# Optimization experiments

Hardware: AMD Instinct MI355X
Metric: run time of the kernel (lower is better)

## Reference

```python
import jax, jax.numpy as jnp
import numpy as np

N = 50000      # nodes
E = 500000     # edges
IN = 256       # input feature dim
HID = 64       # hidden (per-head) dim, layer 1
H1 = 4         # heads, layer 1
NC = 64        # num_classes (layer 2 out, 1 head)
ED = 32        # edge_dim
T = 8          # num_etypes
SLOPE = 0.2    # leakyrelu negative slope


def setup_inputs() -> dict:
    key = jax.random.key(0)
    ks = jax.random.split(key, 20)
    p = lambda k, shape: (jax.random.normal(k, shape, jnp.float32) * 0.05)
    return {
        "h": jax.random.normal(ks[0], (N, IN), jnp.float32),
        "row": jax.random.randint(ks[1], (E,), 0, N, jnp.int32),   # src
        "col": jax.random.randint(ks[2], (E,), 0, N, jnp.int32),   # dst
        "etype": jax.random.randint(ks[3], (E,), 0, T, jnp.int32),
        # layer 1 (4 heads, no residual, elu activation)
        "edge_emb1": p(ks[4], (T, ED)),
        "W1": p(ks[5], (IN, HID * H1)),
        "Wr1": p(ks[6], (T, ED, ED * H1)),      # TypedLinear per-etype weight
        "a_l1": p(ks[7], (H1, HID)),
        "a_r1": p(ks[8], (H1, HID)),
        "a_e1": p(ks[9], (H1, ED)),
        # layer 2 (1 head, residual Linear, no activation)
        "edge_emb2": p(ks[10], (T, ED)),
        "W2": p(ks[11], (HID * H1, NC)),
        "Wr2": p(ks[12], (T, ED, ED)),
        "a_l2": p(ks[13], (1, NC)),
        "a_r2": p(ks[14], (1, NC)),
        "a_e2": p(ks[15], (1, ED)),
        "res_W2": p(ks[16], (HID * H1, NC)),
        "res_b2": p(ks[17], (NC,)),
    }


def _simple_hgn_conv(h, row, col, etype, edge_emb, W, Wr, a_l, a_r, a_e,
                     res_W, res_b, apply_act):
    """One SimpleHGNConv layer. h:[N,in], returns [N, out_dim*H] (D-major, H-minor
    layout, matching emb.permute(0,2,1).view in the torch code)."""
    H, D = a_l.shape            # num_heads, out_dim
    n = h.shape[0]
    emb = (h @ W).reshape(n, H, D)                     # [N,H,D]
    emb = jnp.where(jnp.isnan(emb), 0.0, emb)
    # TypedLinear: edge_emb[etype] @ Wr[etype]; only T distinct rows -> per-type GEMM
    ee = jnp.einsum('te,teo->to', edge_emb, Wr).reshape(T, H, ED)  # [T,H,ED]
    h_l = jnp.einsum('nhd,hd->nh', emb, a_l)[row]      # [E,H]
    h_r = jnp.einsum('nhd,hd->nh', emb, a_r)[col]      # [E,H]
    h_e = jnp.einsum('thd,hd->th', ee, a_e)[etype]     # [E,H]
    att = jax.nn.leaky_relu(h_l + h_r + h_e, SLOPE)    # [E,H]
    # edge_softmax: normalize over incoming edges of each destination node (col)
    seg_max = jax.ops.segment_max(att, col, num_segments=n)   # [N,H]
    att = jnp.exp(att - seg_max[col])
    seg_sum = jax.ops.segment_sum(att, col, num_segments=n)   # [N,H]
    alpha = att / seg_sum[col]                          # [E,H]
    # u_mul_e + sum aggregation
    msg = emb[row] * alpha[:, :, None]                  # [E,H,D]
    out = jax.ops.segment_sum(msg, col, num_segments=n) # [N,H,D]
    out = out.transpose(0, 2, 1).reshape(n, D * H)      # D-major layout
    if res_W is not None:
        out = out + h @ res_W + res_b
    if apply_act:
        out = jax.nn.elu(out)
    return out


def reference(h, row, col, etype,
              edge_emb1, W1, Wr1, a_l1, a_r1, a_e1,
              edge_emb2, W2, Wr2, a_l2, a_r2, a_e2, res_W2, res_b2):
    h1 = _simple_hgn_conv(h, row, col, etype, edge_emb1, W1, Wr1,
                          a_l1, a_r1, a_e1, None, None, True)
    h2 = _simple_hgn_conv(h1, row, col, etype, edge_emb2, W2, Wr2,
                          a_l2, a_r2, a_e2, res_W2, res_b2, False)
    # split by node type (first half type 'l', second half type 'v')
    return (h2[: N // 2], h2[N // 2 :])
```

## Files before the change

### kernel.cpp

```cpp
#include <hip/hip_runtime.h>
#include <hip/hip_bf16.h>

typedef __bf16 bf16x8 __attribute__((ext_vector_type(8)));
typedef float f32x4 __attribute__((ext_vector_type(4)));

#define IN_DIM 256
#define NT 8

__device__ __forceinline__ float b2f(unsigned short u) {
  union { unsigned int i; float f; } x; x.i = ((unsigned int)u) << 16; return x.f;
}
__device__ __forceinline__ float lo2f(unsigned int w) {
  union { unsigned int i; float f; } x; x.i = w << 16; return x.f;
}
__device__ __forceinline__ float hi2f(unsigned int w) {
  union { unsigned int i; float f; } x; x.i = w & 0xFFFF0000u; return x.f;
}
__device__ __forceinline__ unsigned short f2b(float f) {
  union { float f; unsigned int i; } u; u.f = f;
  unsigned int r = u.i + 0x7FFF + ((u.i >> 16) & 1);
  return (unsigned short)(r >> 16);
}
__device__ __forceinline__ float lrelu(float x) { return x >= 0.f ? x : 0.2f * x; }
__device__ __forceinline__ float ldf(const void* p, size_t i, int isf32) {
  return isf32 ? ((const float*)p)[i] : b2f(((const unsigned short*)p)[i]);
}

__global__ void detect_kernel(const unsigned int* __restrict__ hw, int* __restrict__ flag) {
  int tid = threadIdx.x;
  int bad = 0;
  for (int i = 0; i < 4; i++) {
    unsigned int w = hw[tid * 4 + i];
    unsigned int e = (w & 0x7FFFu) >> 7;
    if (e >= 0xC0u) bad++;
  }
#pragma unroll
  for (int off = 32; off; off >>= 1) bad += __shfl_xor(bad, off);
  if (tid == 0) *flag = (bad > 8) ? 1 : 0;
}

__global__ void prep_all_kernel(const void* __restrict__ W1, const void* __restrict__ W2,
                                const void* __restrict__ rW2,
                                const void* __restrict__ al1, const void* __restrict__ ar1,
                                const void* __restrict__ al2, const void* __restrict__ ar2,
                                const void* __restrict__ ee1, const void* __restrict__ Wr1,
                                const void* __restrict__ ae1,
                                const void* __restrict__ ee2, const void* __restrict__ Wr2,
                                const void* __restrict__ ae2,
                                unsigned short* __restrict__ W1t,
                                unsigned short* __restrict__ W2t,
                                float* __restrict__ a2l, float* __restrict__ a2r,
                                float* __restrict__ he1, float* __restrict__ he2,
                                float* __restrict__ alD, float* __restrict__ arD,
                                const int* __restrict__ dflag) {
  int isf32 = *dflag;
  int b = blockIdx.x, tid = threadIdx.x;
  if (b < 384) {
    int j = b, k = tid;
    if (j < 256) {
      int src = (j & 3) * 64 + (j >> 2);
      W1t[j * 256 + k] = f2b(ldf(W1, (size_t)k * 256 + src, isf32));
    } else {
      int o = j - 256;
      float v = (o < 64) ? ldf(W2, (size_t)k * 64 + o, isf32)
                         : ldf(rW2, (size_t)k * 64 + (o - 64), isf32);
      W2t[o * 256 + k] = f2b(v);
    }
  } else if (b < 448) {
    int k = (b - 384) * 4 + (tid >> 6), d = tid & 63;
    float w2 = ldf(W2, (size_t)k * 64 + d, isf32);
    float l2 = w2 * ldf(al2, d, isf32);
    float r2 = w2 * ldf(ar2, d, isf32);
#pragma unroll
    for (int off = 32; off; off >>= 1) { l2 += __shfl_xor(l2, off); r2 += __shfl_xor(r2, off); }
    if (d == 0) { a2l[k] = l2; a2r[k] = r2; }
  } else {
    int bid = b - 448;
    int t = tid >> 5, d = tid & 31;
    if (bid < 4) {
      int h = bid;
      float s = 0.f;
#pragma unroll
      for (int e = 0; e < 32; e++)
        s += ldf(ee1, t * 32 + e, isf32) * ldf(Wr1, (size_t)(t * 32 + e) * 128 + h * 32 + d, isf32);
      float v = s * ldf(ae1, h * 32 + d, isf32);
#pragma unroll
      for (int off = 16; off; off >>= 1) v += __shfl_xor(v, off);
      if (d == 0) he1[t * 4 + h] = v;
    } else if (bid == 4) {
      float s = 0.f;
#pragma unroll
      for (int e = 0; e < 32; e++)
        s += ldf(ee2, t * 32 + e, isf32) * ldf(Wr2, (size_t)(t * 32 + e) * 32 + d, isf32);
      float v = s * ldf(ae2, d, isf32);
#pragma unroll
      for (int off = 16; off; off >>= 1) v += __shfl_xor(v, off);
      if (d == 0) he2[t] = v;
    } else {
      int j = tid;
      alD[j] = ldf(al1, (j & 3) * 64 + (j >> 2), isf32);
      arD[j] = ldf(ar1, (j & 3) * 64 + (j >> 2), isf32);
    }
  }
}

__global__ __launch_bounds__(256, 2) void gemm1_fused(
    const void* __restrict__ A, int M,
    const unsigned short* __restrict__ Bt,
    unsigned short* __restrict__ emb1,
    const float* __restrict__ alD, const float* __restrict__ arD,
    float* __restrict__ hl1, float* __restrict__ hr1,
    const int* __restrict__ dflag) {
  __shared__ unsigned short As[64 * 64];
  __shared__ unsigned short Bs[256 * 64];
  __shared__ float lsum[4][64][4];
  __shared__ float rsum[4][64][4];
  int isf32 = *dflag;
  const int tid = threadIdx.x;
  const int m0 = blockIdx.x * 64;
  const int wv = tid >> 6, lane = tid & 63;
  const int q = lane >> 4, m = lane & 15;
  const int jp = wv * 64;
  f32x4 acc[4][4] = {};
  for (int kc = 0; kc < 256; kc += 64) {
    {
      int row = tid >> 2, qt = tid & 3;
      int gr = m0 + row;
      unsigned short tmp[16];
      if (gr < M) {
        if (isf32) {
          const float* ap = (const float*)A + (size_t)gr * 256 + kc + qt * 16;
          float4 v0 = *(const float4*)ap;
          float4 v1 = *(const float4*)(ap + 4);
          float4 v2 = *(const float4*)(ap + 8);
          float4 v3 = *(const float4*)(ap + 12);
          tmp[0]=f2b(v0.x); tmp[1]=f2b(v0.y); tmp[2]=f2b(v0.z); tmp[3]=f2b(v0.w);
          tmp[4]=f2b(v1.x); tmp[5]=f2b(v1.y); tmp[6]=f2b(v1.z); tmp[7]=f2b(v1.w);
          tmp[8]=f2b(v2.x); tmp[9]=f2b(v2.y); tmp[10]=f2b(v2.z); tmp[11]=f2b(v2.w);
          tmp[12]=f2b(v3.x); tmp[13]=f2b(v3.y); tmp[14]=f2b(v3.z); tmp[15]=f2b(v3.w);
        } else {
          const unsigned short* ap = (const unsigned short*)A + (size_t)gr * 256 + kc + qt * 16;
          *(int4*)tmp = *(const int4*)ap;
          *(int4*)(tmp + 8) = *(const int4*)(ap + 8);
        }
      } else {
        for (int x = 0; x < 16; x++) tmp[x] = 0;
      }
      int g0 = (qt * 2) ^ (row & 7);
      int g1 = (qt * 2 + 1) ^ (row & 7);
      *(int4*)(As + row * 64 + g0 * 8) = *(int4*)tmp;
      *(int4*)(As + row * 64 + g1 * 8) = *(int4*)(tmp + 8);
    }
    {
#pragma unroll
      for (int i = 0; i < 8; i++) {
        int id = tid + i * 256;
        int row = id >> 3, gg = id & 7;
        int4 v = *(const int4*)(Bt + (size_t)row * 256 + kc + gg * 8);
        int pg = gg ^ (row & 7);
        *(int4*)(Bs + row * 64 + pg * 8) = v;
      }
    }
    __syncthreads();
#pragma unroll
    for (int ks = 0; ks < 2; ks++) {
      int gk = ks * 4 + q;
      bf16x8 afr[4];
#pragma unroll
      for (int cm = 0; cm < 4; cm++) {
        int row = cm * 16 + m;
        afr[cm] = *(const bf16x8*)(As + row * 64 + (gk ^ (row & 7)) * 8);
      }
#pragma unroll
      for (int cj = 0; cj < 4; cj++) {
        int jr = jp + cj * 16 + m;
        bf16x8 b = *(const bf16x8*)(Bs + jr * 64 + (gk ^ (jr & 7)) * 8);
#pragma unroll
        for (int cm = 0; cm < 4; cm++)
          acc[cm][cj] = __builtin_amdgcn_mfma_f32_16x16x32_bf16(afr[cm], b, acc[cm][cj], 0, 0, 0);
      }
    }
    __syncthreads();
  }
  float al[4], ar[4];
#pragma unroll
  for (int cj = 0; cj < 4; cj++) {
    al[cj] = alD[jp + cj * 16 + m];
    ar[cj] = arD[jp + cj * 16 + m];
  }
#pragma unroll
  for (int cm = 0; cm < 4; cm++) {
#pragma unroll
    for (int r = 0; r < 4; r++) {
      int lrow = cm * 16 + q * 4 + r;
      int gm = m0 + lrow;
      float lp = 0.f, rp = 0.f;
#pragma unroll
      for (int cj = 0; cj < 4; cj++) {
        float v = acc[cm][cj][r];
        if (gm < M) emb1[(size_t)gm * 256 + jp + cj * 16 + m] = f2b(v);
        lp += v * al[cj]; rp += v * ar[cj];
      }
      lp += __shfl_xor(lp, 4); lp += __shfl_xor(lp, 8);
      rp += __shfl_xor(rp, 4); rp += __shfl_xor(rp, 8);
      if (m < 4) { lsum[wv][lrow][m] = lp; rsum[wv][lrow][m] = rp; }
    }
  }
  __syncthreads();
  {
    int row = tid >> 2, h = tid & 3;
    int gm = m0 + row;
    if (gm < M) {
      float l = lsum[0][row][h] + lsum[1][row][h] + lsum[2][row][h] + lsum[3][row][h];
      float r = rsum[0][row][h] + rsum[1][row][h] + rsum[2][row][h] + rsum[3][row][h];
      hl1[(size_t)gm * 4 + h] = l;
      hr1[(size_t)gm * 4 + h] = r;
    }
  }
}

__global__ __launch_bounds__(256, 2) void gemm2_fused(
    const unsigned short* __restrict__ A, int M,
    const unsigned short* __restrict__ Bt,
    unsigned short* __restrict__ emb2, unsigned short* __restrict__ res,
    const void* __restrict__ bias, const int* __restrict__ dflag) {
  __shared__ unsigned short As[64 * 64];
  __shared__ unsigned short Bs[128 * 64];
  int isf32 = *dflag;
  const int tid = threadIdx.x;
  const int m0 = blockIdx.x * 64;
  const int wv = tid >> 6, lane = tid & 63;
  const int q = lane >> 4, m = lane & 15;
  const int jp = (wv & 1) * 64;
  const int mh = (wv >> 1) * 32;
  f32x4 acc[2][4] = {};
  for (int kc = 0; kc < 256; kc += 64) {
    {
      int row = tid >> 2, qt = tid & 3;
      int gr = m0 + row;
      unsigned short tmp[16];
      if (gr < M) {
        const unsigned short* ap = A + (size_t)gr * 256 + kc + qt * 16;
        *(int4*)tmp = *(const int4*)ap;
        *(int4*)(tmp + 8) = *(const int4*)(ap + 8);
      } else {
        for (int x = 0; x < 16; x++) tmp[x] = 0;
      }
      int g0 = (qt * 2) ^ (row & 7);
      int g1 = (qt * 2 + 1) ^ (row & 7);
      *(int4*)(As + row * 64 + g0 * 8) = *(int4*)tmp;
      *(int4*)(As + row * 64 + g1 * 8) = *(int4*)(tmp + 8);
    }
    {
#pragma unroll
      for (int i = 0; i < 4; i++) {
        int id = tid + i * 256;
        int row = id >> 3, gg = id & 7;
        int4 v = *(const int4*)(Bt + (size_t)row * 256 + kc + gg * 8);
        int pg = gg ^ (row & 7);
        *(int4*)(Bs + row * 64 + pg * 8) = v;
      }
    }
    __syncthreads();
#pragma unroll
    for (int ks = 0; ks < 2; ks++) {
      int gk = ks * 4 + q;
      bf16x8 afr[2];
#pragma unroll
      for (int cm = 0; cm < 2; cm++) {
        int row = mh + cm * 16 + m;
        afr[cm] = *(const bf16x8*)(As + row * 64 + (gk ^ (row & 7)) * 8);
      }
#pragma unroll
      for (int cj = 0; cj < 4; cj++) {
        int jr = jp + cj * 16 + m;
        bf16x8 b = *(const bf16x8*)(Bs + jr * 64 + (gk ^ (jr & 7)) * 8);
#pragma unroll
        for (int cm = 0; cm < 2; cm++)
          acc[cm][cj] = __builtin_amdgcn_mfma_f32_16x16x32_bf16(afr[cm], b, acc[cm][cj], 0, 0, 0);
      }
    }
    __syncthreads();
  }
  float bv[4];
#pragma unroll
  for (int cj = 0; cj < 4; cj++)
    bv[cj] = (jp == 64) ? ldf(bias, cj * 16 + m, isf32) : 0.f;
#pragma unroll
  for (int cm = 0; cm < 2; cm++) {
#pragma unroll
    for (int r = 0; r < 4; r++) {
      int gm = m0 + mh + cm * 16 + q * 4 + r;
      if (gm < M) {
#pragma unroll
        for (int cj = 0; cj < 4; cj++) {
          float v = acc[cm][cj][r];
          int gj = cj * 16 + m;
          if (jp == 0) emb2[(size_t)gm * 64 + gj] = f2b(v);
          else res[(size_t)gm * 64 + gj] = f2b(v + bv[cj]);
        }
      }
    }
  }
}

__global__ void count_kernel(const int* __restrict__ col, int* __restrict__ cnt,
                             int E_, int N_) {
  int e = blockIdx.x * 256 + threadIdx.x;
  if (e >= E_) return;
  int c = col[e];
  if ((unsigned)c < (unsigned)N_) atomicAdd(&cnt[c], 1);
}

__global__ void scan1_kernel(const int* __restrict__ cnt, int* __restrict__ ptrb,
                             int* __restrict__ bsum, int n) {
  __shared__ int wsum[4];
  int tid = threadIdx.x, lane = tid & 63, wid = tid >> 6;
  int i = blockIdx.x * 256 + tid;
  int v = (i < n) ? cnt[i] : 0;
  int x = v;
#pragma unroll
  for (int off = 1; off < 64; off <<= 1) {
    int y = __shfl_up(x, off);
    if (lane >= off) x += y;
  }
  if (lane == 63) wsum[wid] = x;
  __syncthreads();
  int woff = 0;
#pragma unroll
  for (int k = 0; k < 4; k++) woff += (k < wid) ? wsum[k] : 0;
  if (i < n) ptrb[i] = x - v + woff;
  if (tid == 255) bsum[blockIdx.x] = woff + x;
}

__global__ void scan2_kernel(int* __restrict__ bsum, int* __restrict__ ptrb,
                             int nb, int n) {
  __shared__ int wsum[4];
  int tid = threadIdx.x, lane = tid & 63, wid = tid >> 6;
  int v = (tid < nb) ? bsum[tid] : 0;
  int x = v;
#pragma unroll
  for (int off = 1; off < 64; off <<= 1) {
    int y = __shfl_up(x, off);
    if (lane >= off) x += y;
  }
  if (lane == 63) wsum[wid] = x;
  __syncthreads();
  int woff = 0;
#pragma unroll
  for (int k = 0; k < 4; k++) woff += (k < wid) ? wsum[k] : 0;
  if (tid < nb) bsum[tid] = x - v + woff;
  if (tid == 255) ptrb[n] = woff + x;
}

__global__ void scan3_kernel(int* __restrict__ ptrb, const int* __restrict__ bsum, int n) {
  int i = blockIdx.x * 256 + threadIdx.x;
  if (i < n) ptrb[i] += bsum[blockIdx.x];
}

__global__ void fill_kernel(const int* __restrict__ col, const int* __restrict__ row,
                            const int* __restrict__ ety, const int* __restrict__ ptrb,
                            int* __restrict__ cnt, int* __restrict__ srcc, int E_, int N_) {
  int e = blockIdx.x * 256 + threadIdx.x;
  if (e >= E_) return;
  int c = col[e];
  if ((unsigned)c >= (unsigned)N_) return;
  int pos = atomicSub(&cnt[c], 1) - 1;
  long long slot = (long long)ptrb[c] + pos;
  if (slot >= 0 && slot < E_) {
    int sr = row[e], t = ety[e];
    srcc[slot] = ((unsigned)sr < (unsigned)N_ && (unsigned)t < (unsigned)NT)
                     ? (sr | (t << 20)) : -1;
  }
}

__global__ __launch_bounds__(256) void agg1_kernel(
    const int* __restrict__ ptrb, const int* __restrict__ srcc,
    const float* __restrict__ hl1, const float* __restrict__ hr1,
    const float* __restrict__ he1,
    const unsigned short* __restrict__ emb1, unsigned short* __restrict__ h1,
    const float* __restrict__ a2l, const float* __restrict__ a2r,
    float* __restrict__ hl2, float* __restrict__ hr2,
    int N_, int E_) {
  __shared__ float4 wds[4][64];
  __shared__ int sds[4][64];
  int wv = threadIdx.x >> 6, lane = threadIdx.x & 63;
  int node = blockIdx.x * 4 + wv;
  if (node >= N_) return;
  int p0 = ptrb[node], p1 = ptrb[node + 1];
  p0 = max(0, min(p0, E_)); p1 = max(p0, min(p1, E_));
  float4 hrv = *(const float4*)(hr1 + 4 * (size_t)node);
  float s0 = 0.f, s1 = 0.f, s2 = 0.f, s3 = 0.f;
  float acc[8] = {0.f,0.f,0.f,0.f,0.f,0.f,0.f,0.f};
  int g = lane >> 5, sub = lane & 31;
  for (int pb = p0; pb < p1; pb += 64) {
    int mc = p1 - pb; if (mc > 64) mc = 64;
    float4 w = {0.f, 0.f, 0.f, 0.f};
    int src = 0;
    if (lane < mc) {
      int spk = srcc[pb + lane];
      if (spk >= 0) {
        int sr = spk & 0xFFFFF, t = spk >> 20;
        float4 a = *(const float4*)(hl1 + 4 * (size_t)sr);
        float4 gg = *(const float4*)(he1 + 4 * (size_t)t);
        w.x = __expf(lrelu(a.x + hrv.x + gg.x));
        w.y = __expf(lrelu(a.y + hrv.y + gg.y));
        w.z = __expf(lrelu(a.z + hrv.z + gg.z));
        w.w = __expf(lrelu(a.w + hrv.w + gg.w));
        src = sr;
      }
    }
    s0 += w.x; s1 += w.y; s2 += w.z; s3 += w.w;
    wds[wv][lane] = w;
    sds[wv][lane] = src;
    for (int j = 0; j < mc; j += 4) {
      int jj0 = j + g, jj1 = j + 2 + g;
      bool v0 = jj0 < mc, v1 = jj1 < mc;
      float4 u0, u1; int r0 = 0, r1 = 0;
      int4 raw0, raw1;
      if (v0) { u0 = wds[wv][jj0]; r0 = sds[wv][jj0];
                raw0 = *(const int4*)(emb1 + (size_t)r0 * 256 + sub * 8); }
      if (v1) { u1 = wds[wv][jj1]; r1 = sds[wv][jj1];
                raw1 = *(const int4*)(emb1 + (size_t)r1 * 256 + sub * 8); }
      if (v0) {
        acc[0] += u0.x * lo2f(raw0.x); acc[1] += u0.y * hi2f(raw0.x);
        acc[2] += u0.z * lo2f(raw0.y); acc[3] += u0.w * hi2f(raw0.y);
        acc[4] += u0.x * lo2f(raw0.z); acc[5] += u0.y * hi2f(raw0.z);
        acc[6] += u0.z * lo2f(raw0.w); acc[7] += u0.w * hi2f(raw0.w);
      }
      if (v1) {
        acc[0] += u1.x * lo2f(raw1.x); acc[1] += u1.y * hi2f(raw1.x);
        acc[2] += u1.z * lo2f(raw1.y); acc[3] += u1.w * hi2f(raw1.y);
        acc[4] += u1.x * lo2f(raw1.z); acc[5] += u1.y * hi2f(raw1.z);
        acc[6] += u1.z * lo2f(raw1.w); acc[7] += u1.w * hi2f(raw1.w);
      }
    }
  }
#pragma unroll
  for (int off = 32; off; off >>= 1) {
    s0 += __shfl_xor(s0, off); s1 += __shfl_xor(s1, off);
    s2 += __shfl_xor(s2, off); s3 += __shfl_xor(s3, off);
  }
#pragma unroll
  for (int k = 0; k < 8; k++) acc[k] += __shfl_xor(acc[k], 32);
  float lp = 0.f, rp = 0.f;
  if (g == 0) {
    float sv[4] = {s0, s1, s2, s3};
    unsigned short o[8];
#pragma unroll
    for (int k = 0; k < 8; k++) {
      float r = (sv[k & 3] > 0.f) ? acc[k] / sv[k & 3] : 0.f;
      r = r > 0.f ? r : __expf(r) - 1.f;
      o[k] = f2b(r);
      int j = sub * 8 + k;
      lp += r * a2l[j];
      rp += r * a2r[j];
    }
    *(int4*)(h1 + (size_t)node * 256 + sub * 8) = *(int4*)o;
  }
#pragma unroll
  for (int off = 1; off < 32; off <<= 1) { lp += __shfl_xor(lp, off); rp += __shfl_xor(rp, off); }
  if (lane == 0) { hl2[node] = lp; hr2[node] = rp; }
}

__global__ __launch_bounds__(256) void agg2_kernel(
    const int* __restrict__ ptrb, const int* __restrict__ srcc,
    const float* __restrict__ hl2, const float* __restrict__ hr2,
    const float* __restrict__ he2,
    const unsigned short* __restrict__ emb2, const unsigned short* __restrict__ res,
    void* __restrict__ out, int N_, int E_, const int* __restrict__ dflag) {
  __shared__ int2 wsd[4][64];
  int isf32 = *dflag;
  int wv = threadIdx.x >> 6, lane = threadIdx.x & 63;
  int node = blockIdx.x * 4 + wv;
  if (node >= N_) return;
  int p0 = ptrb[node], p1 = ptrb[node + 1];
  p0 = max(0, min(p0, E_)); p1 = max(p0, min(p1, E_));
  float hrv = hr2[node];
  float s = 0.f;
  float acc[4] = {0.f, 0.f, 0.f, 0.f};
  int g = lane >> 4, sub = lane & 15;
  for (int pb = p0; pb < p1; pb += 64) {
    int mc = p1 - pb; if (mc > 64) mc = 64;
    float w = 0.f;
    int src = 0;
    if (lane < mc) {
      int spk = srcc[pb + lane];
      if (spk >= 0) {
        int sr = spk & 0xFFFFF, t = spk >> 20;
        w = __expf(lrelu(hl2[sr] + hrv + he2[t]));
        src = sr;
      }
    }
    s += w;
    int2 pk; pk.x = __float_as_int(w); pk.y = src;
    wsd[wv][lane] = pk;
    for (int j = 0; j < mc; j += 8) {
      int jj0 = j + g, jj1 = j + 4 + g;
      bool v0 = jj0 < mc, v1 = jj1 < mc;
      float u0, u1; int r0 = 0, r1 = 0;
      int2 raw0, raw1;
      if (v0) { int2 ws = wsd[wv][jj0]; u0 = __int_as_float(ws.x); r0 = ws.y;
                raw0 = *(const int2*)(emb2 + (size_t)r0 * 64 + sub * 4); }
      if (v1) { int2 ws = wsd[wv][jj1]; u1 = __int_as_float(ws.x); r1 = ws.y;
                raw1 = *(const int2*)(emb2 + (size_t)r1 * 64 + sub * 4); }
      if (v0) {
        acc[0] += u0 * lo2f(raw0.x); acc[1] += u0 * hi2f(raw0.x);
        acc[2] += u0 * lo2f(raw0.y); acc[3] += u0 * hi2f(raw0.y);
      }
      if (v1) {
        acc[0] += u1 * lo2f(raw1.x); acc[1] += u1 * hi2f(raw1.x);
        acc[2] += u1 * lo2f(raw1.y); acc[3] += u1 * hi2f(raw1.y);
      }
    }
  }
#pragma unroll
  for (int off = 32; off; off >>= 1) s += __shfl_xor(s, off);
#pragma unroll
  for (int k = 0; k < 4; k++) {
    acc[k] += __shfl_xor(acc[k], 16);
    acc[k] += __shfl_xor(acc[k], 32);
  }
  if (g == 0) {
    ushort4 rv = *(const ushort4*)(res + (size_t)node * 64 + sub * 4);
    float o0 = ((s > 0.f) ? acc[0] / s : 0.f) + b2f(rv.x);
    float o1 = ((s > 0.f) ? acc[1] / s : 0.f) + b2f(rv.y);
    float o2 = ((s > 0.f) ? acc[2] / s : 0.f) + b2f(rv.z);
    float o3 = ((s > 0.f) ? acc[3] / s : 0.f) + b2f(rv.w);
    size_t oi = (size_t)node * 64 + sub * 4;
    if (isf32) {
      float4 ov = {o0, o1, o2, o3};
      *(float4*)((float*)out + oi) = ov;
    } else {
      ushort4 ov; ov.x = f2b(o0); ov.y = f2b(o1); ov.z = f2b(o2); ov.w = f2b(o3);
      *(ushort4*)((unsigned short*)out + oi) = ov;
    }
  }
}

extern "C" void kernel_launch(void* const* d_in, const int* in_sizes, int n_in,
                              void* d_out, int out_size, void* d_ws, size_t ws_size,
                              hipStream_t stream) {
  const int N = in_sizes[0] / IN_DIM;
  const int E = in_sizes[1];

  const void* h   = d_in[0];
  const int* row  = (const int*)d_in[1];
  const int* col  = (const int*)d_in[2];
  const int* ety  = (const int*)d_in[3];
  const void* ee1 = d_in[4];
  const void* W1  = d_in[5];
  const void* Wr1 = d_in[6];
  const void* al1 = d_in[7];
  const void* ar1 = d_in[8];
  const void* ae1 = d_in[9];
  const void* ee2 = d_in[10];
  const void* W2  = d_in[11];
  const void* Wr2 = d_in[12];
  const void* al2 = d_in[13];
  const void* ar2 = d_in[14];
  const void* ae2 = d_in[15];
  const void* rW2 = d_in[16];
  const void* rb2 = d_in[17];

  char* p = (char*)d_ws;
  auto take = [&](size_t b) { char* q = p; p += (b + 255) & ~(size_t)255; return q; };
  unsigned short* h1   = (unsigned short*)take((size_t)N * 256 * 2);
  unsigned short* emb1 = (unsigned short*)take((size_t)N * 256 * 2);
  int* srcc = (int*)take((size_t)E * 4);
  int* ptrb = (int*)take((size_t)(N + 1) * 4);
  int* cnt  = (int*)take((size_t)N * 4);
  int* bsum = (int*)take(1024);
  float* hl1 = (float*)take((size_t)N * 4 * 4);
  float* hr1 = (float*)take((size_t)N * 4 * 4);
  float* hl2 = (float*)take((size_t)N * 4);
  float* hr2 = (float*)take((size_t)N * 4);
  unsigned short* W1t = (unsigned short*)take(256 * 256 * 2);
  unsigned short* W2t = (unsigned short*)take(128 * 256 * 2);
  float* a2l = (float*)take(256 * 4);
  float* a2r = (float*)take(256 * 4);
  float* alD = (float*)take(256 * 4);
  float* arD = (float*)take(256 * 4);
  float* he1 = (float*)take(NT * 4 * 4);
  float* he2 = (float*)take(NT * 4);
  int* dflag = (int*)take(256);
  unsigned short* emb2 = emb1;
  unsigned short* res  = emb1 + (size_t)N * 64;

  const size_t need = (size_t)(p - (char*)d_ws);
  if (need > ws_size) {
    hipMemsetAsync(d_out, 0, (size_t)out_size * 2, stream);
    return;
  }

  const int EB = (E + 255) / 256;
  const int MB = (N + 63) / 64;
  const int SB = (N + 255) / 256;

  detect_kernel<<<1, 64, 0, stream>>>((const unsigned int*)h, dflag);
  hipMemsetAsync(cnt, 0, (size_t)N * 4, stream);
  prep_all_kernel<<<454, 256, 0, stream>>>(W1, W2, rW2, al1, ar1, al2, ar2,
                                           ee1, Wr1, ae1, ee2, Wr2, ae2,
                                           W1t, W2t, a2l, a2r, he1, he2, alD, arD, dflag);

  count_kernel<<<EB, 256, 0, stream>>>(col, cnt, E, N);
  scan1_kernel<<<SB, 256, 0, stream>>>(cnt, ptrb, bsum, N);
  scan2_kernel<<<1, 256, 0, stream>>>(bsum, ptrb, SB, N);
  scan3_kernel<<<SB, 256, 0, stream>>>(ptrb, bsum, N);
  fill_kernel<<<EB, 256, 0, stream>>>(col, row, ety, ptrb, cnt, srcc, E, N);

  gemm1_fused<<<MB, 256, 0, stream>>>(h, N, W1t, emb1, alD, arD, hl1, hr1, dflag);
  agg1_kernel<<<(N + 3) / 4, 256, 0, stream>>>(
      ptrb, srcc, hl1, hr1, he1, emb1, h1, a2l, a2r, hl2, hr2, N, E);

  gemm2_fused<<<MB, 256, 0, stream>>>(h1, N, W2t, emb2, res, rb2, dflag);
  agg2_kernel<<<(N + 3) / 4, 256, 0, stream>>>(
      ptrb, srcc, hl2, hr2, he2, emb2, res, d_out, N, E, dflag);
}
```

Baseline: 284.5 us.

## Map four destination nodes per wavefront in both aggregation kernels

Both aggregation kernels now assign 16 lanes per destination node, so one wavefront handles four nodes instead of one. This targets the lane waste seen with average degree around 10, where most of a 64-wide edge chunk sat idle, and drops the cross-half shuffle reductions. Each lane now gathers 32 bytes of bf16 per edge in agg1 and keeps 16 accumulators. In exchange, register pressure rises and nodes in the same wave with unequal degree cause divergence through the __any loop.

```diff
diff --git a/kernel.cpp b/kernel.cpp
--- a/kernel.cpp
+++ b/kernel.cpp
@@ -384,83 +384,121 @@
     int N_, int E_) {
   __shared__ float4 wds[4][64];
   __shared__ int sds[4][64];
-  int wv = threadIdx.x >> 6, lane = threadIdx.x & 63;
-  int node = blockIdx.x * 4 + wv;
-  if (node >= N_) return;
-  int p0 = ptrb[node], p1 = ptrb[node + 1];
-  p0 = max(0, min(p0, E_)); p1 = max(p0, min(p1, E_));
-  float4 hrv = *(const float4*)(hr1 + 4 * (size_t)node);
+  const int tid = threadIdx.x;
+  const int wv = tid >> 6, lane = tid & 63;
+  const int g = lane >> 4, ln = lane & 15;
+  const int node = blockIdx.x * 16 + wv * 4 + g;
+  const bool nv = node < N_;
+  int p0 = 0, p1 = 0;
+  if (nv) {
+    p0 = ptrb[node]; p1 = ptrb[node + 1];
+    p0 = max(0, min(p0, E_)); p1 = max(p0, min(p1, E_));
+  }
+  float4 hrv = {0.f, 0.f, 0.f, 0.f};
+  if (nv) hrv = *(const float4*)(hr1 + 4 * (size_t)node);
   float s0 = 0.f, s1 = 0.f, s2 = 0.f, s3 = 0.f;
-  float acc[8] = {0.f,0.f,0.f,0.f,0.f,0.f,0.f,0.f};
-  int g = lane >> 5, sub = lane & 31;
-  for (int pb = p0; pb < p1; pb += 64) {
-    int mc = p1 - pb; if (mc > 64) mc = 64;
+  float acc[16];
+#pragma unroll
+  for (int k = 0; k < 16; k++) acc[k] = 0.f;
+  const unsigned short* erow = emb1 + ln * 16;
+  for (int pb = p0;; pb += 16) {
+    if (!__any(pb < p1)) break;
+    int mc = (pb < p1) ? min(p1 - pb, 16) : 0;
     float4 w = {0.f, 0.f, 0.f, 0.f};
     int src = 0;
-    if (lane < mc) {
-      int spk = srcc[pb + lane];
+    if (ln < mc) {
+      int spk = srcc[pb + ln];
       if (spk >= 0) {
         int sr = spk & 0xFFFFF, t = spk >> 20;
         float4 a = *(const float4*)(hl1 + 4 * (size_t)sr);
-        float4 gg = *(const float4*)(he1 + 4 * (size_t)t);
-        w.x = __expf(lrelu(a.x + hrv.x + gg.x));
-        w.y = __expf(lrelu(a.y + hrv.y + gg.y));
-        w.z = __expf(lrelu(a.z + hrv.z + gg.z));
-        w.w = __expf(lrelu(a.w + hrv.w + gg.w));
+        float4 ge = *(const float4*)(he1 + 4 * (size_t)t);
+        w.x = __expf(lrelu(a.x + hrv.x + ge.x));
+        w.y = __expf(lrelu(a.y + hrv.y + ge.y));
+        w.z = __expf(lrelu(a.z + hrv.z + ge.z));
+        w.w = __expf(lrelu(a.w + hrv.w + ge.w));
         src = sr;
       }
     }
     s0 += w.x; s1 += w.y; s2 += w.z; s3 += w.w;
     wds[wv][lane] = w;
     sds[wv][lane] = src;
-    for (int j = 0; j < mc; j += 4) {
-      int jj0 = j + g, jj1 = j + 2 + g;
-      bool v0 = jj0 < mc, v1 = jj1 < mc;
-      float4 u0, u1; int r0 = 0, r1 = 0;
-      int4 raw0, raw1;
-      if (v0) { u0 = wds[wv][jj0]; r0 = sds[wv][jj0];
-                raw0 = *(const int4*)(emb1 + (size_t)r0 * 256 + sub * 8); }
-      if (v1) { u1 = wds[wv][jj1]; r1 = sds[wv][jj1];
-                raw1 = *(const int4*)(emb1 + (size_t)r1 * 256 + sub * 8); }
-      if (v0) {
-        acc[0] += u0.x * lo2f(raw0.x); acc[1] += u0.y * hi2f(raw0.x);
-        acc[2] += u0.z * lo2f(raw0.y); acc[3] += u0.w * hi2f(raw0.y);
-        acc[4] += u0.x * lo2f(raw0.z); acc[5] += u0.y * hi2f(raw0.z);
-        acc[6] += u0.z * lo2f(raw0.w); acc[7] += u0.w * hi2f(raw0.w);
-      }
+    for (int j = 0; j < mc; j += 2) {
+      bool v1 = (j + 1) < mc;
+      float4 u0 = wds[wv][g * 16 + j];
+      int r0 = sds[wv][g * 16 + j];
+      const unsigned short* e0 = erow + (size_t)r0 * 256;
+      int4 ra = *(const int4*)e0;
+      int4 rb = *(const int4*)(e0 + 8);
+      float4 u1; int4 rc, rd;
       if (v1) {
-        acc[0] += u1.x * lo2f(raw1.x); acc[1] += u1.y * hi2f(raw1.x);
-        acc[2] += u1.z * lo2f(raw1.y); acc[3] += u1.w * hi2f(raw1.y);
-        acc[4] += u1.x * lo2f(raw1.z); acc[5] += u1.y * hi2f(raw1.z);
-        acc[6] += u1.z * lo2f(raw1.w); acc[7] += u1.w * hi2f(raw1.w);
-      }
-    }
-  }
-#pragma unroll
-  for (int off = 32; off; off >>= 1) {
+        u1 = wds[wv][g * 16 + j + 1];
+        int r1 = sds[wv][g * 16 + j + 1];
+        const unsigned short* e1 = erow + (size_t)r1 * 256;
+        rc = *(const int4*)e1;
+        rd = *(const int4*)(e1 + 8);
+      }
+      acc[0]  += u0.x * lo2f(ra.x); acc[1]  += u0.y * hi2f(ra.x);
+      acc[2]  += u0.z * lo2f(ra.y); acc[3]  += u0.w * hi2f(ra.y);
+      acc[4]  += u0.x * lo2f(ra.z); acc[5]  += u0.y * hi2f(ra.z);
+      acc[6]  += u0.z * lo2f(ra.w); acc[7]  += u0.w * hi2f(ra.w);
+      acc[8]  += u0.x * lo2f(rb.x); acc[9]  += u0.y * hi2f(rb.x);
+      acc[10] += u0.z * lo2f(rb.y); acc[11] += u0.w * hi2f(rb.y);
+      acc[12] += u0.x * lo2f(rb.z); acc[13] += u0.y * hi2f(rb.z);
+      acc[14] += u0.z * lo2f(rb.w); acc[15] += u0.w * hi2f(rb.w);
+      if (v1) {
+        acc[0]  += u1.x * lo2f(rc.x); acc[1]  += u1.y * hi2f(rc.x);
+        acc[2]  += u1.z * lo2f(rc.y); acc[3]  += u1.w * hi2f(rc.y);
+        acc[4]  += u1.x * lo2f(rc.z); acc[5]  += u1.y * hi2f(rc.z);
+        acc[6]  += u1.z * lo2f(rc.w); acc[7]  += u1.w * hi2f(rc.w);
+        acc[8]  += u1.x * lo2f(rd.x); acc[9]  += u1.y * hi2f(rd.x);
+        acc[10] += u1.z * lo2f(rd.y); acc[11] += u1.w * hi2f(rd.y);
+        acc[12] += u1.x * lo2f(rd.z); acc[13] += u1.y * hi2f(rd.z);
+        acc[14] += u1.z * lo2f(rd.w); acc[15] += u1.w * hi2f(rd.w);
+      }
+    }
+  }
+#pragma unroll
+  for (int off = 1; off < 16; off <<= 1) {
     s0 += __shfl_xor(s0, off); s1 += __shfl_xor(s1, off);
     s2 += __shfl_xor(s2, off); s3 += __shfl_xor(s3, off);
   }
-#pragma unroll
-  for (int k = 0; k < 8; k++) acc[k] += __shfl_xor(acc[k], 32);
+  float invs[4];
+  invs[0] = s0 > 0.f ? 1.f / s0 : 0.f;
+  invs[1] = s1 > 0.f ? 1.f / s1 : 0.f;
+  invs[2] = s2 > 0.f ? 1.f / s2 : 0.f;
+  invs[3] = s3 > 0.f ? 1.f / s3 : 0.f;
+  float alv[16], arv[16];
+#pragma unroll
+  for (int q2 = 0; q2 < 4; q2++) {
+    float4 t1 = *(const float4*)(a2l + ln * 16 + q2 * 4);
+    float4 t2 = *(const float4*)(a2r + ln * 16 + q2 * 4);
+    alv[q2 * 4 + 0] = t1.x; alv[q2 * 4 + 1] = t1.y;
+    alv[q2 * 4 + 2] = t1.z; alv[q2 * 4 + 3] = t1.w;
+    arv[q2 * 4 + 0] = t2.x; arv[q2 * 4 + 1] = t2.y;
+    arv[q2 * 4 + 2] = t2.z; arv[q2 * 4 + 3] = t2.w;
+  }
   float lp = 0.f, rp = 0.f;
-  if (g == 0) {
-    float sv[4] = {s0, s1, s2, s3};
-    unsigned short o[8];
-#pragma unroll
-    for (int k = 0; k < 8; k++) {
-      float r = (sv[k & 3] > 0.f) ? acc[k] / sv[k & 3] : 0.f;
-      r = r > 0.f ? r : __expf(r) - 1.f;
-      o[k] = f2b(r);
-      int j = sub * 8 + k;
-      lp += r * a2l[j];
-      rp += r * a2r[j];
-    }
-    *(int4*)(h1 + (size_t)node * 256 + sub * 8) = *(int4*)o;
-  }
-#pragma unroll
-  for (int off = 1; off < 32; off <<= 1) { lp += __shfl_xor(lp, off); rp += __shfl_xor(rp, off); }
-  if (lane == 0) { hl2[node] = lp; hr2[node] = rp; }
+  unsigned int ow[8];
+#pragma unroll
+  for (int k = 0; k < 16; k++) {
+    float r = acc[k] * invs[k & 3];
+    r = r > 0.f ? r : __expf(r) - 1.f;
+    unsigned int bb = f2b(r);
+    if ((k & 1) == 0) ow[k >> 1] = bb; else ow[k >> 1] |= bb << 16;
+    lp += r * alv[k];
+    rp += r * arv[k];
+  }
+  if (nv) {
+    int4 va; va.x = ow[0]; va.y = ow[1]; va.z = ow[2]; va.w = ow[3];
+    int4 vb; vb.x = ow[4]; vb.y = ow[5]; vb.z = ow[6]; vb.w = ow[7];
+    *(int4*)(h1 + (size_t)node * 256 + ln * 16) = va;
+    *(int4*)(h1 + (size_t)node * 256 + ln * 16 + 8) = vb;
+  }
+#pragma unroll
+  for (int off = 1; off < 16; off <<= 1) {
+    lp += __shfl_xor(lp, off); rp += __shfl_xor(rp, off);
+  }
+  if (nv && ln == 0) { hl2[node] = lp; hr2[node] = rp; }
 }
 
 __global__ __launch_bounds__(256) void agg2_kernel(
@@ -470,22 +508,27 @@
     const unsigned short* __restrict__ emb2, const unsigned short* __restrict__ res,
     void* __restrict__ out, int N_, int E_, const int* __restrict__ dflag) {
   __shared__ int2 wsd[4][64];
-  int isf32 = *dflag;
-  int wv = threadIdx.x >> 6, lane = threadIdx.x & 63;
-  int node = blockIdx.x * 4 + wv;
-  if (node >= N_) return;
-  int p0 = ptrb[node], p1 = ptrb[node + 1];
-  p0 = max(0, min(p0, E_)); p1 = max(p0, min(p1, E_));
-  float hrv = hr2[node];
+  const int isf32 = *dflag;
+  const int tid = threadIdx.x;
+  const int wv = tid >> 6, lane = tid & 63;
+  const int g = lane >> 4, ln = lane & 15;
+  const int node = blockIdx.x * 16 + wv * 4 + g;
+  const bool nv = node < N_;
+  int p0 = 0, p1 = 0;
+  if (nv) {
+    p0 = ptrb[node]; p1 = ptrb[node + 1];
+    p0 = max(0, min(p0, E_)); p1 = max(p0, min(p1, E_));
+  }
+  float hrv = nv ? hr2[node] : 0.f;
   float s = 0.f;
   float acc[4] = {0.f, 0.f, 0.f, 0.f};
-  int g = lane >> 4, sub = lane & 15;
-  for (int pb = p0; pb < p1; pb += 64) {
-    int mc = p1 - pb; if (mc > 64) mc = 64;
-    float w = 0.f;
-    int src = 0;
-    if (lane < mc) {
-      int spk = srcc[pb + lane];
+  const unsigned short* erow = emb2 + ln * 4;
+  for (int pb = p0;; pb += 16) {
+    if (!__any(pb < p1)) break;
+    int mc = (pb < p1) ? min(p1 - pb, 16) : 0;
+    float w = 0.f; int src = 0;
+    if (ln < mc) {
+      int spk = srcc[pb + ln];
       if (spk >= 0) {
         int sr = spk & 0xFFFFF, t = spk >> 20;
         w = __expf(lrelu(hl2[sr] + hrv + he2[t]));
@@ -495,39 +538,35 @@
     s += w;
     int2 pk; pk.x = __float_as_int(w); pk.y = src;
     wsd[wv][lane] = pk;
-    for (int j = 0; j < mc; j += 8) {
-      int jj0 = j + g, jj1 = j + 4 + g;
-      bool v0 = jj0 < mc, v1 = jj1 < mc;
-      float u0, u1; int r0 = 0, r1 = 0;
-      int2 raw0, raw1;
-      if (v0) { int2 ws = wsd[wv][jj0]; u0 = __int_as_float(ws.x); r0 = ws.y;
-                raw0 = *(const int2*)(emb2 + (size_t)r0 * 64 + sub * 4); }
-      if (v1) { int2 ws = wsd[wv][jj1]; u1 = __int_as_float(ws.x); r1 = ws.y;
-                raw1 = *(const int2*)(emb2 + (size_t)r1 * 64 + sub * 4); }
-      if (v0) {
-        acc[0] += u0 * lo2f(raw0.x); acc[1] += u0 * hi2f(raw0.x);
-        acc[2] += u0 * lo2f(raw0.y); acc[3] += u0 * hi2f(raw0.y);
-      }
+    for (int j = 0; j < mc; j += 2) {
+      bool v1 = (j + 1) < mc;
+      int2 w0 = wsd[wv][g * 16 + j];
+      float u0 = __int_as_float(w0.x);
+      int2 ra = *(const int2*)(erow + (size_t)w0.y * 64);
+      float u1 = 0.f; int2 rc;
       if (v1) {
-        acc[0] += u1 * lo2f(raw1.x); acc[1] += u1 * hi2f(raw1.x);
-        acc[2] += u1 * lo2f(raw1.y); acc[3] += u1 * hi2f(raw1.y);
-      }
-    }
-  }
-#pragma unroll
-  for (int off = 32; off; off >>= 1) s += __shfl_xor(s, off);
-#pragma unroll
-  for (int k = 0; k < 4; k++) {
-    acc[k] += __shfl_xor(acc[k], 16);
-    acc[k] += __shfl_xor(acc[k], 32);
-  }
-  if (g == 0) {
-    ushort4 rv = *(const ushort4*)(res + (size_t)node * 64 + sub * 4);
-    float o0 = ((s > 0.f) ? acc[0] / s : 0.f) + b2f(rv.x);
-    float o1 = ((s > 0.f) ? acc[1] / s : 0.f) + b2f(rv.y);
-    float o2 = ((s > 0.f) ? acc[2] / s : 0.f) + b2f(rv.z);
-    float o3 = ((s > 0.f) ? acc[3] / s : 0.f) + b2f(rv.w);
-    size_t oi = (size_t)node * 64 + sub * 4;
+        int2 w1 = wsd[wv][g * 16 + j + 1];
+        u1 = __int_as_float(w1.x);
+        rc = *(const int2*)(erow + (size_t)w1.y * 64);
+      }
+      acc[0] += u0 * lo2f(ra.x); acc[1] += u0 * hi2f(ra.x);
+      acc[2] += u0 * lo2f(ra.y); acc[3] += u0 * hi2f(ra.y);
+      if (v1) {
+        acc[0] += u1 * lo2f(rc.x); acc[1] += u1 * hi2f(rc.x);
+        acc[2] += u1 * lo2f(rc.y); acc[3] += u1 * hi2f(rc.y);
+      }
+    }
+  }
+#pragma unroll
+  for (int off = 1; off < 16; off <<= 1) s += __shfl_xor(s, off);
+  float inv = s > 0.f ? 1.f / s : 0.f;
+  if (nv) {
+    ushort4 rv = *(const ushort4*)(res + (size_t)node * 64 + ln * 4);
+    float o0 = acc[0] * inv + b2f(rv.x);
+    float o1 = acc[1] * inv + b2f(rv.y);
+    float o2 = acc[2] * inv + b2f(rv.z);
+    float o3 = acc[3] * inv + b2f(rv.w);
+    size_t oi = (size_t)node * 64 + ln * 4;
     if (isf32) {
       float4 ov = {o0, o1, o2, o3};
       *(float4*)((float*)out + oi) = ov;
@@ -596,6 +635,7 @@
   const int EB = (E + 255) / 256;
   const int MB = (N + 63) / 64;
   const int SB = (N + 255) / 256;
+  const int AB = (N + 15) / 16;
 
   detect_kernel<<<1, 64, 0, stream>>>((const unsigned int*)h, dflag);
   hipMemsetAsync(cnt, 0, (size_t)N * 4, stream);
@@ -610,10 +650,10 @@
   fill_kernel<<<EB, 256, 0, stream>>>(col, row, ety, ptrb, cnt, srcc, E, N);
 
   gemm1_fused<<<MB, 256, 0, stream>>>(h, N, W1t, emb1, alD, arD, hl1, hr1, dflag);
-  agg1_kernel<<<(N + 3) / 4, 256, 0, stream>>>(
+  agg1_kernel<<<AB, 256, 0, stream>>>(
       ptrb, srcc, hl1, hr1, he1, emb1, h1, a2l, a2r, hl2, hr2, N, E);
 
   gemm2_fused<<<MB, 256, 0, stream>>>(h1, N, W2t, emb2, res, rb2, dflag);
-  agg2_kernel<<<(N + 3) / 4, 256, 0, stream>>>(
+  agg2_kernel<<<AB, 256, 0, stream>>>(
       ptrb, srcc, hl2, hr2, he2, emb2, res, d_out, N, E, dflag);
 }
```

Measured after the change: 273.6 us. -3.8%, faster.
